# Kernel tuning notes

Hardware: AMD Instinct MI355X
Metric: run time of the kernel (lower is better)

Reference implementation:

```python
import jax, jax.numpy as jnp
import numpy as np

DIM = 1024
CTX_DIM = 1024
HEADS = 16
DIM_HEAD = 64
INNER = HEADS * DIM_HEAD
SCALE = DIM_HEAD ** -0.5


def _layer_norm(x, g, b, eps=1e-5):
    mu = x.mean(-1, keepdims=True)
    var = ((x - mu) ** 2).mean(-1, keepdims=True)
    return (x - mu) * jax.lax.rsqrt(var + eps) * g + b


def setup_inputs() -> dict:
    key = jax.random.key(0)
    ks = jax.random.split(key, 10)
    b, i, j = 2, 1024, 1024
    s = lambda fan_in: 1.0 / np.sqrt(fan_in)
    return {
        "x": jax.random.normal(ks[0], (b, i, DIM), jnp.float32),
        "context": jax.random.normal(ks[1], (b, j, CTX_DIM), jnp.float32),
        "mask": jnp.ones((b, i), dtype=bool),
        "context_mask": jnp.ones((b, j), dtype=bool),
        "ln_g": jnp.ones((DIM,), jnp.float32),
        "ln_b": jnp.zeros((DIM,), jnp.float32),
        "cln_g": jnp.ones((CTX_DIM,), jnp.float32),
        "cln_b": jnp.zeros((CTX_DIM,), jnp.float32),
        "W_qk": jax.random.normal(ks[2], (DIM, INNER), jnp.float32) * s(DIM),
        "W_cqk": jax.random.normal(ks[3], (CTX_DIM, INNER), jnp.float32) * s(CTX_DIM),
        "W_v": jax.random.normal(ks[4], (DIM, INNER), jnp.float32) * s(DIM),
        "W_cv": jax.random.normal(ks[5], (CTX_DIM, INNER), jnp.float32) * s(CTX_DIM),
        "W_out": jax.random.normal(ks[6], (INNER, DIM), jnp.float32) * s(INNER),
        "b_out": jnp.zeros((DIM,), jnp.float32),
        "W_cout": jax.random.normal(ks[7], (INNER, CTX_DIM), jnp.float32) * s(INNER),
        "b_cout": jnp.zeros((CTX_DIM,), jnp.float32),
        "W_th": jax.random.normal(ks[8], (HEADS, HEADS), jnp.float32) * s(HEADS),   # talking heads [out_h, in_h]
        "W_cth": jax.random.normal(ks[9], (HEADS, HEADS), jnp.float32) * s(HEADS),
    }


def reference(x, context, mask, context_mask, ln_g, ln_b, cln_g, cln_b,
              W_qk, W_cqk, W_v, W_cv, W_out, b_out, W_cout, b_cout, W_th, W_cth):
    b, i, _ = x.shape
    j = context.shape[1]
    xn = _layer_norm(x, ln_g, ln_b)
    cn = _layer_norm(context, cln_g, cln_b)

    split = lambda t: t.reshape(t.shape[0], t.shape[1], HEADS, DIM_HEAD).transpose(0, 2, 1, 3)  # b h n d
    qk = split(xn @ W_qk)
    cqk = split(cn @ W_cqk)
    v = split(xn @ W_v)
    cv = split(cn @ W_cv)

    sim = jnp.einsum('bhid,bhjd->bhij', qk, cqk) * SCALE

    attn_mask = mask[:, None, :, None] & context_mask[:, None, None, :]  # b 1 i j
    sim = jnp.where(attn_mask, sim, -jnp.finfo(sim.dtype).max)

    attn = jax.nn.softmax(sim, axis=-1)       # rows: x attends to context
    cattn = jax.nn.softmax(sim, axis=-2)      # cols: context attends to x

    # talking heads: 1x1 conv over head dim, weight [out_h, in_h]
    attn = jnp.einsum('bhij,gh->bgij', attn, W_th)
    cattn = jnp.einsum('bhij,gh->bgij', cattn, W_cth)

    out = jnp.einsum('bhij,bhjd->bhid', attn, cv)
    cout = jnp.einsum('bhji,bhjd->bhid', cattn, v)

    merge = lambda t: t.transpose(0, 2, 1, 3).reshape(t.shape[0], t.shape[2], INNER)
    out = merge(out) @ W_out + b_out
    cout = merge(cout) @ W_cout + b_cout
    return out, cout
```

## Files before the change

kernel.cpp:

```cpp
#include <hip/hip_runtime.h>
#include <hip/hip_bf16.h>

#define BB 2
#define SEQ 1024
#define DIMD 1024
#define NH 16
#define DH 64
#define INNERD 1024
#define SCALEF 0.125f

typedef __hip_bfloat16 bf16;
typedef __attribute__((ext_vector_type(8))) short short8;
typedef __attribute__((ext_vector_type(4))) float f32x4;

__device__ __forceinline__ float b2f(bf16 x) { return __bfloat162float(x); }
__device__ __forceinline__ bf16 f2b(float x) { return __float2bfloat16(x); }
__device__ __forceinline__ float s2f(unsigned short s) {
    return __uint_as_float(((unsigned int)s) << 16);
}
__device__ __forceinline__ unsigned short f2bs(float v) {
    bf16 t = __float2bfloat16(v);
    return *(unsigned short*)&t;
}

__device__ __forceinline__ void stf(float* p, size_t i, float v) { p[i] = v; }
__device__ __forceinline__ void stf(bf16* p, size_t i, float v) { p[i] = f2b(v); }

__device__ __forceinline__ void async16(const short* g, short* l) {
    __builtin_amdgcn_global_load_lds(
        (const __attribute__((address_space(1))) unsigned int*)(g),
        (__attribute__((address_space(3))) unsigned int*)(l), 16, 0, 0);
}

__global__ __launch_bounds__(256) void ln2_kernel(const float* __restrict__ x0,
                                                  const float* __restrict__ g0,
                                                  const float* __restrict__ b0,
                                                  bf16* __restrict__ o0,
                                                  const float* __restrict__ x1,
                                                  const float* __restrict__ g1,
                                                  const float* __restrict__ b1,
                                                  bf16* __restrict__ o1) {
    int rowg = blockIdx.x;
    int sel = rowg >= BB * SEQ;
    int row = sel ? rowg - BB * SEQ : rowg;
    const float* xr = (sel ? x1 : x0) + (size_t)row * DIMD;
    const float* g = sel ? g1 : g0;
    const float* b = sel ? b1 : b0;
    bf16* orow = (sel ? o1 : o0) + (size_t)row * DIMD;
    int tid = threadIdx.x;
    float v[4];
    float s = 0.f, s2 = 0.f;
#pragma unroll
    for (int k = 0; k < 4; ++k) {
        v[k] = xr[tid + k * 256];
        s += v[k];
        s2 += v[k] * v[k];
    }
    __shared__ float sh1[256], sh2[256];
    sh1[tid] = s; sh2[tid] = s2;
    __syncthreads();
    for (int off = 128; off > 0; off >>= 1) {
        if (tid < off) { sh1[tid] += sh1[tid + off]; sh2[tid] += sh2[tid + off]; }
        __syncthreads();
    }
    float mu = sh1[0] * (1.f / DIMD);
    float var = sh2[0] * (1.f / DIMD) - mu * mu;
    float rstd = rsqrtf(var + 1e-5f);
#pragma unroll
    for (int k = 0; k < 4; ++k) {
        int c = tid + k * 256;
        orow[c] = f2b((v[k] - mu) * rstd * g[c] + b[c]);
    }
}

__global__ __launch_bounds__(256) void transpose_w6(
    const float* __restrict__ s0, const float* __restrict__ s1,
    const float* __restrict__ s2, const float* __restrict__ s3,
    const float* __restrict__ s4, const float* __restrict__ s5,
    bf16* __restrict__ d0, bf16* __restrict__ d1, bf16* __restrict__ d2,
    bf16* __restrict__ d3, bf16* __restrict__ d4, bf16* __restrict__ d5) {
    int z = blockIdx.z;
    const float* W = z == 0 ? s0 : z == 1 ? s1 : z == 2 ? s2 : z == 3 ? s3
                     : z == 4 ? s4 : s5;
    bf16* Wt = z == 0 ? d0 : z == 1 ? d1 : z == 2 ? d2 : z == 3 ? d3
               : z == 4 ? d4 : d5;
    __shared__ float T[32][33];
    int n0 = blockIdx.x * 32, k0 = blockIdx.y * 32;
    int tx = threadIdx.x & 31, ty = threadIdx.x >> 5;
#pragma unroll
    for (int s = 0; s < 4; ++s)
        T[ty + s * 8][tx] = W[(size_t)(k0 + ty + s * 8) * 1024 + n0 + tx];
    __syncthreads();
#pragma unroll
    for (int s = 0; s < 4; ++s)
        Wt[(size_t)(n0 + ty + s * 8) * 1024 + k0 + tx] = f2b(T[tx][ty + s * 8]);
}

__global__ __launch_bounds__(256) void transpose_v2(const bf16* __restrict__ sA,
                                                    bf16* __restrict__ dA,
                                                    const bf16* __restrict__ sB,
                                                    bf16* __restrict__ dB) {
    __shared__ short T[32][34];
    int z = blockIdx.z;
    int sel = z >> 5, bh = z & 31;
    int b = bh >> 4, h = bh & 15;
    const bf16* src = sel ? sB : sA;
    bf16* dst = sel ? dB : dA;
    int n0 = blockIdx.x * 32, d0 = blockIdx.y * 32;
    int tx = threadIdx.x & 31, ty = threadIdx.x >> 5;
    const short* s = (const short*)(src + (size_t)b * SEQ * INNERD + h * DH);
    short* d = (short*)(dst + (size_t)bh * DH * SEQ);
#pragma unroll
    for (int k = 0; k < 4; ++k)
        T[ty + k * 8][tx] = s[(size_t)(n0 + ty + k * 8) * INNERD + d0 + tx];
    __syncthreads();
#pragma unroll
    for (int k = 0; k < 4; ++k)
        d[(size_t)(d0 + ty + k * 8) * SEQ + n0 + tx] = T[tx][ty + k * 8];
}

template <typename TC, bool HASBIAS, int BM, int BN, int MT, int NT, int ZS>
__global__ __launch_bounds__(256) void mfma_gemm(
    const bf16* __restrict__ A, long sA1, long sA2, int lda,
    const bf16* __restrict__ Bt, long sB1, long sB2, int ldb,
    TC* __restrict__ C, long sC1, long sC2, int ldc,
    const float* __restrict__ bias0, const float* __restrict__ bias1,
    float alpha, int K) {
    constexpr int WX = BN / (NT * 16);
    static_assert((4 / WX) * MT * 16 == BM, "BM/waves mismatch");
    static_assert(BM % 64 == 0 && BN % 64 == 0, "chunk uniformity");
    int z = blockIdx.z;
    int zb = z / ZS, zh = z % ZS;
    const short* Ag = (const short*)(A + zb * sA1 + zh * sA2);
    const short* Bg = (const short*)(Bt + zb * sB1 + zh * sB2);
    TC* Cp = C + zb * sC1 + zh * sC2;
    const float* bias = (zh == 0) ? bias0 : bias1;

    const int m0 = blockIdx.y * BM;
    const int n0 = blockIdx.x * BN;
    int tid = threadIdx.x;
    int wave = tid >> 6, lane = tid & 63;
    int wm = (wave / WX) * (MT * 16), wn = (wave % WX) * (NT * 16);
    int lrow = lane & 15, lquad = lane >> 4;

    __shared__ short S[(BM + BN) * 32];

    f32x4 acc[MT][NT] = {};

    for (int k0 = 0; k0 < K; k0 += 32) {
        constexpr int CH = (BM + BN) / 64;
#pragma unroll
        for (int ch = 0; ch < CH; ++ch) {
            int e = ch * 256 + tid;
            int r = e >> 2, c = (e & 3) * 8;
            const short* g = (r < BM)
                                 ? Ag + (size_t)(m0 + r) * lda + k0 + c
                                 : Bg + (size_t)(n0 + r - BM) * ldb + k0 + c;
            async16(g, S + (size_t)e * 8);
        }
        __syncthreads();
        short8 af[MT], bfv[NT];
#pragma unroll
        for (int mt = 0; mt < MT; ++mt)
            af[mt] = *(const short8*)(S + (wm + mt * 16 + lrow) * 32 + lquad * 8);
#pragma unroll
        for (int nt = 0; nt < NT; ++nt)
            bfv[nt] = *(const short8*)(S + (BM + wn + nt * 16 + lrow) * 32 + lquad * 8);
#pragma unroll
        for (int mt = 0; mt < MT; ++mt)
#pragma unroll
            for (int nt = 0; nt < NT; ++nt)
                acc[mt][nt] = __builtin_amdgcn_mfma_f32_16x16x32_bf16(
                    af[mt], bfv[nt], acc[mt][nt], 0, 0, 0);
        __syncthreads();
    }
#pragma unroll
    for (int mt = 0; mt < MT; ++mt) {
#pragma unroll
        for (int nt = 0; nt < NT; ++nt) {
            int col = n0 + wn + nt * 16 + lrow;
#pragma unroll
            for (int r = 0; r < 4; ++r) {
                int row = m0 + wm + mt * 16 + lquad * 4 + r;
                float v = acc[mt][nt][r] * alpha;
                if (HASBIAS) v += bias[col];
                stf(Cp, (size_t)row * ldc + col, v);
            }
        }
    }
}

__global__ __launch_bounds__(256) void qkt_stats_kernel(
    const bf16* __restrict__ qk, const bf16* __restrict__ cqk,
    bf16* __restrict__ sim16, float* __restrict__ rowPart,
    float* __restrict__ colPart, long sQ, long sS, long sP) {
    int z = blockIdx.z;
    int b = z >> 4, h = z & 15;
    const short* Ag = (const short*)(qk + b * sQ + h * DH);
    const short* Bg = (const short*)(cqk + b * sQ + h * DH);
    bf16* Cp = sim16 + b * sS + (size_t)h * SEQ * SEQ;
    rowPart += b * sP;
    colPart += b * sP;

    const int m0 = blockIdx.y * 128;
    const int n0 = blockIdx.x * 128;
    int tid = threadIdx.x;
    int wave = tid >> 6, lane = tid & 63;
    int wy = wave >> 1, wx = wave & 1;
    int wm = wy * 64, wn = wx * 64;
    int lrow = lane & 15, lquad = lane >> 4;

    __shared__ short S[256 * 32];
    __shared__ float rowLDS[128][2];
    __shared__ float colLDS[128][2];

    f32x4 acc[4][4] = {};

    for (int k0 = 0; k0 < DH; k0 += 32) {
#pragma unroll
        for (int ch = 0; ch < 4; ++ch) {
            int e = ch * 256 + tid;
            int r = e >> 2, c = (e & 3) * 8;
            const short* g = (r < 128)
                                 ? Ag + (size_t)(m0 + r) * INNERD + k0 + c
                                 : Bg + (size_t)(n0 + r - 128) * INNERD + k0 + c;
            async16(g, S + (size_t)e * 8);
        }
        __syncthreads();
        short8 af[4], bfv[4];
#pragma unroll
        for (int mt = 0; mt < 4; ++mt)
            af[mt] = *(const short8*)(S + (wm + mt * 16 + lrow) * 32 + lquad * 8);
#pragma unroll
        for (int nt = 0; nt < 4; ++nt)
            bfv[nt] = *(const short8*)(S + (128 + wn + nt * 16 + lrow) * 32 + lquad * 8);
#pragma unroll
        for (int mt = 0; mt < 4; ++mt)
#pragma unroll
            for (int nt = 0; nt < 4; ++nt)
                acc[mt][nt] = __builtin_amdgcn_mfma_f32_16x16x32_bf16(
                    af[mt], bfv[nt], acc[mt][nt], 0, 0, 0);
        __syncthreads();
    }
    float rband[16];
    float cacc[4] = {};
#pragma unroll
    for (int k = 0; k < 16; ++k) rband[k] = 0.f;
#pragma unroll
    for (int mt = 0; mt < 4; ++mt) {
#pragma unroll
        for (int nt = 0; nt < 4; ++nt) {
            int col = n0 + wn + nt * 16 + lrow;
#pragma unroll
            for (int r = 0; r < 4; ++r) {
                int row = m0 + wm + mt * 16 + lquad * 4 + r;
                unsigned short us = f2bs(acc[mt][nt][r] * SCALEF);
                *((unsigned short*)Cp + (size_t)row * SEQ + col) = us;
                float e = __expf(s2f(us));
                rband[mt * 4 + r] += e;
                cacc[nt] += e;
            }
        }
    }
#pragma unroll
    for (int m = 1; m < 16; m <<= 1)
#pragma unroll
        for (int k = 0; k < 16; ++k) rband[k] += __shfl_xor(rband[k], m, 64);
    if (lrow == 0) {
#pragma unroll
        for (int mt = 0; mt < 4; ++mt)
#pragma unroll
            for (int r = 0; r < 4; ++r)
                rowLDS[wm + mt * 16 + lquad * 4 + r][wx] = rband[mt * 4 + r];
    }
#pragma unroll
    for (int m = 16; m < 64; m <<= 1)
#pragma unroll
        for (int nt = 0; nt < 4; ++nt) cacc[nt] += __shfl_xor(cacc[nt], m, 64);
    if (lquad == 0) {
#pragma unroll
        for (int nt = 0; nt < 4; ++nt)
            colLDS[wn + nt * 16 + lrow][wy] = cacc[nt];
    }
    __syncthreads();
    if (tid < 128)
        rowPart[((size_t)h * 8 + blockIdx.x) * SEQ + m0 + tid] =
            rowLDS[tid][0] + rowLDS[tid][1];
    else
        colPart[((size_t)h * 8 + blockIdx.y) * SEQ + n0 + tid - 128] =
            colLDS[tid - 128][0] + colLDS[tid - 128][1];
}

__global__ __launch_bounds__(256) void finish_inv2_kernel(const float* __restrict__ partA,
                                                          float* __restrict__ invA,
                                                          const float* __restrict__ partB,
                                                          float* __restrict__ invB) {
    int idx = blockIdx.x * 256 + threadIdx.x;
    int h = idx >> 10, t = idx & 1023;
    float sA = 0.f, sB = 0.f;
#pragma unroll
    for (int p = 0; p < 8; ++p) {
        sA += partA[((size_t)h * 8 + p) * SEQ + t];
        sB += partB[((size_t)h * 8 + p) * SEQ + t];
    }
    invA[idx] = 1.f / sA;
    invB[idx] = 1.f / sB;
}

__global__ __launch_bounds__(256) void mix_kernel(bf16* simattn,
                                                  bf16* __restrict__ catT,
                                                  const float* __restrict__ rli,
                                                  const float* __restrict__ cli,
                                                  const float* __restrict__ Wth,
                                                  const float* __restrict__ Wcth) {
    int d = blockIdx.y * gridDim.x + blockIdx.x;
    int grp = d >> 4, s = d & 15;
    int pairIdx = grp * 8 + (s & 7);
    int half = s >> 3;
    int j0 = (2 * (pairIdx & 31) + half) * 16;
    int i0 = (pairIdx >> 5) * 16;
    int tid = threadIdx.x;
    int jl = tid & 15, il = tid >> 4;
    int i = i0 + il, j = j0 + jl;
    float sa[16] = {}, sc[16] = {};
#pragma unroll
    for (int h = 0; h < 16; ++h) {
        float s2 = b2f(simattn[((size_t)h * SEQ + i) * SEQ + j]);
        float e = __expf(s2);
        float p = e * rli[h * SEQ + i];
        float q = e * cli[h * SEQ + j];
#pragma unroll
        for (int g = 0; g < 16; ++g) {
            sa[g] += p * Wth[g * 16 + h];
            sc[g] += q * Wcth[g * 16 + h];
        }
    }
#pragma unroll
    for (int g = 0; g < 16; ++g)
        simattn[((size_t)g * SEQ + i) * SEQ + j] = f2b(sa[g]);
    __shared__ float T[16][16][17];
#pragma unroll
    for (int g = 0; g < 16; ++g) T[g][il][jl] = sc[g];
    __syncthreads();
#pragma unroll
    for (int g = 0; g < 16; ++g)
        catT[((size_t)g * SEQ + j0 + il) * SEQ + i0 + jl] = f2b(T[g][jl][il]);
}

extern "C" void kernel_launch(void* const* d_in, const int* in_sizes, int n_in,
                              void* d_out, int out_size, void* d_ws, size_t ws_size,
                              hipStream_t stream) {
    const float* x = (const float*)d_in[0];
    const float* ctx = (const float*)d_in[1];
    const float* ln_g = (const float*)d_in[4];
    const float* ln_b = (const float*)d_in[5];
    const float* cln_g = (const float*)d_in[6];
    const float* cln_b = (const float*)d_in[7];
    const float* W_qk = (const float*)d_in[8];
    const float* W_cqk = (const float*)d_in[9];
    const float* W_v = (const float*)d_in[10];
    const float* W_cv = (const float*)d_in[11];
    const float* W_out = (const float*)d_in[12];
    const float* b_out = (const float*)d_in[13];
    const float* W_cout = (const float*)d_in[14];
    const float* b_cout = (const float*)d_in[15];
    const float* W_th = (const float*)d_in[16];
    const float* W_cth = (const float*)d_in[17];
    float* out = (float*)d_out;

    char* ws = (char*)d_ws;
    size_t off = 0;
    auto alloc = [&](size_t bytes) {
        void* p = ws + off;
        off += (bytes + 255) & ~(size_t)255;
        return p;
    };
    const size_t NTOK = (size_t)BB * SEQ * DIMD;
    const size_t WSZ = (size_t)DIMD * INNERD;
    const size_t U = (size_t)NH * SEQ * SEQ;
    const long HB = (long)NH * DH * SEQ;

    bf16* xn = (bf16*)alloc(NTOK * 2);
    bf16* cn = (bf16*)alloc(NTOK * 2);
    bf16* qk = (bf16*)alloc(NTOK * 2);
    bf16* vv = (bf16*)alloc(NTOK * 2);
    bf16* cqk = (bf16*)alloc(NTOK * 2);
    bf16* cv = (bf16*)alloc(NTOK * 2);
    bf16* wqk_t = (bf16*)alloc(WSZ * 2);
    bf16* wv_t = (bf16*)alloc(WSZ * 2);
    bf16* wcqk_t = (bf16*)alloc(WSZ * 2);
    bf16* wcv_t = (bf16*)alloc(WSZ * 2);
    bf16* wout_t = (bf16*)alloc(WSZ * 2);
    bf16* wcout_t = (bf16*)alloc(WSZ * 2);
    bf16* cvT = (bf16*)alloc(NTOK * 2);
    bf16* vT = (bf16*)alloc(NTOK * 2);
    bf16* outm = xn;

    const size_t partB = (size_t)NH * 8 * SEQ * 4;
    const size_t invB = (size_t)NH * SEQ * 4;
    const size_t bigNeed = 4 * U * 2 + 2 * (2 * partB) + 2 * (2 * invB);
    bool big = (ws_size > off) && (ws_size - off >= bigNeed);

    transpose_w6<<<dim3(32, 32, 6), 256, 0, stream>>>(
        W_qk, W_v, W_cqk, W_cv, W_out, W_cout,
        wqk_t, wv_t, wcqk_t, wcv_t, wout_t, wcout_t);
    ln2_kernel<<<2 * BB * SEQ, 256, 0, stream>>>(x, ln_g, ln_b, xn,
                                                 ctx, cln_g, cln_b, cn);
    mfma_gemm<bf16, false, 128, 64, 2, 4, 2><<<dim3(16, 16, 4), 256, 0, stream>>>(
        xn, (long)NTOK, 0, DIMD,
        wqk_t, (long)(2 * WSZ), (long)WSZ, DIMD,
        qk, (long)(2 * NTOK), (long)NTOK, INNERD,
        nullptr, nullptr, 1.0f, DIMD);
    transpose_v2<<<dim3(32, 2, 64), 256, 0, stream>>>(vv, vT, cv, cvT);

    if (big) {
        bf16* sim0 = (bf16*)alloc(U * 2);
        bf16* sim1 = (bf16*)alloc(U * 2);
        bf16* cb0 = (bf16*)alloc(U * 2);
        bf16* cb1 = (bf16*)alloc(U * 2);
        float* rowPart = (float*)alloc(2 * partB);
        float* colPart = (float*)alloc(2 * partB);
        float* rowInv = (float*)alloc(2 * invB);
        float* colInv = (float*)alloc(2 * invB);

        qkt_stats_kernel<<<dim3(8, 8, 32), 256, 0, stream>>>(
            qk, cqk, sim0, rowPart, colPart,
            (long)SEQ * INNERD, (long)U, (long)NH * 8 * SEQ);
        finish_inv2_kernel<<<2 * NH * SEQ / 256, 256, 0, stream>>>(rowPart, rowInv,
                                                                   colPart, colInv);
        mix_kernel<<<dim3(SEQ / 16, SEQ / 16), 256, 0, stream>>>(
            sim0, cb0, rowInv, colInv, W_th, W_cth);
        mix_kernel<<<dim3(SEQ / 16, SEQ / 16), 256, 0, stream>>>(
            sim1, cb1, rowInv + NH * SEQ, colInv + NH * SEQ, W_th, W_cth);
        mfma_gemm<bf16, false, 64, 64, 1, 4, 16><<<dim3(1, 16, 4 * NH), 256, 0, stream>>>(
            sim0, (long)U, (long)SEQ * SEQ, SEQ,
            cvT, HB, (long)DH * SEQ, SEQ,
            outm, (long)SEQ * INNERD, (long)DH, INNERD,
            nullptr, nullptr, 1.0f, SEQ);
    } else {
        bf16* simA = (bf16*)alloc(U * 2);
        bf16* cbuf = (bf16*)alloc(U * 2);
        float* rowPart = (float*)alloc(partB);
        float* colPart = (float*)alloc(partB);
        float* rowInv = (float*)alloc(invB);
        float* colInv = (float*)alloc(invB);
        for (int b = 0; b < BB; ++b) {
            qkt_stats_kernel<<<dim3(8, 8, 16), 256, 0, stream>>>(
                qk + (size_t)b * SEQ * INNERD, cqk + (size_t)b * SEQ * INNERD,
                simA, rowPart, colPart, 0, 0, 0);
            finish_inv2_kernel<<<NH * SEQ / 256, 256, 0, stream>>>(rowPart, rowInv,
                                                                   colPart, colInv);
            mix_kernel<<<dim3(SEQ / 16, SEQ / 16), 256, 0, stream>>>(
                simA, cbuf, rowInv, colInv, W_th, W_cth);
            mfma_gemm<bf16, false, 64, 64, 1, 4, 16><<<dim3(1, 16, 2 * NH), 256, 0,
                                                       stream>>>(
                simA, (long)U, (long)SEQ * SEQ, SEQ,
                cvT + (size_t)b * HB, (long)NTOK, (long)DH * SEQ, SEQ,
                outm + (size_t)b * SEQ * INNERD, (long)NTOK, (long)DH, INNERD,
                nullptr, nullptr, 1.0f, SEQ);
        }
    }

    mfma_gemm<float, true, 128, 64, 2, 4, 2><<<dim3(16, 16, 2), 256, 0, stream>>>(
        outm, 0, (long)NTOK, INNERD, wout_t, 0, (long)WSZ, INNERD,
        out, 0, (long)NTOK, DIMD, b_out, b_cout, 1.0f, INNERD);
}
```

Before: 295.9 us.

## Merge prep kernels, deepen GEMM K-step to 64, batch mix launches

```diff
diff --git a/kernel.cpp b/kernel.cpp
--- a/kernel.cpp
+++ b/kernel.cpp
@@ -32,68 +32,65 @@
         (__attribute__((address_space(3))) unsigned int*)(l), 16, 0, 0);
 }
 
-__global__ __launch_bounds__(256) void ln2_kernel(const float* __restrict__ x0,
-                                                  const float* __restrict__ g0,
-                                                  const float* __restrict__ b0,
-                                                  bf16* __restrict__ o0,
-                                                  const float* __restrict__ x1,
-                                                  const float* __restrict__ g1,
-                                                  const float* __restrict__ b1,
-                                                  bf16* __restrict__ o1) {
-    int rowg = blockIdx.x;
-    int sel = rowg >= BB * SEQ;
-    int row = sel ? rowg - BB * SEQ : rowg;
-    const float* xr = (sel ? x1 : x0) + (size_t)row * DIMD;
-    const float* g = sel ? g1 : g0;
-    const float* b = sel ? b1 : b0;
-    bf16* orow = (sel ? o1 : o0) + (size_t)row * DIMD;
-    int tid = threadIdx.x;
-    float v[4];
-    float s = 0.f, s2 = 0.f;
-#pragma unroll
-    for (int k = 0; k < 4; ++k) {
-        v[k] = xr[tid + k * 256];
-        s += v[k];
-        s2 += v[k] * v[k];
-    }
-    __shared__ float sh1[256], sh2[256];
-    sh1[tid] = s; sh2[tid] = s2;
-    __syncthreads();
-    for (int off = 128; off > 0; off >>= 1) {
-        if (tid < off) { sh1[tid] += sh1[tid + off]; sh2[tid] += sh2[tid + off]; }
-        __syncthreads();
-    }
-    float mu = sh1[0] * (1.f / DIMD);
-    float var = sh2[0] * (1.f / DIMD) - mu * mu;
-    float rstd = rsqrtf(var + 1e-5f);
-#pragma unroll
-    for (int k = 0; k < 4; ++k) {
-        int c = tid + k * 256;
-        orow[c] = f2b((v[k] - mu) * rstd * g[c] + b[c]);
-    }
-}
-
-__global__ __launch_bounds__(256) void transpose_w6(
+__global__ __launch_bounds__(256) void prep_kernel(
     const float* __restrict__ s0, const float* __restrict__ s1,
     const float* __restrict__ s2, const float* __restrict__ s3,
     const float* __restrict__ s4, const float* __restrict__ s5,
     bf16* __restrict__ d0, bf16* __restrict__ d1, bf16* __restrict__ d2,
-    bf16* __restrict__ d3, bf16* __restrict__ d4, bf16* __restrict__ d5) {
+    bf16* __restrict__ d3, bf16* __restrict__ d4, bf16* __restrict__ d5,
+    const float* __restrict__ x0, const float* __restrict__ g0,
+    const float* __restrict__ b0, bf16* __restrict__ o0,
+    const float* __restrict__ x1, const float* __restrict__ g1,
+    const float* __restrict__ b1, bf16* __restrict__ o1) {
     int z = blockIdx.z;
-    const float* W = z == 0 ? s0 : z == 1 ? s1 : z == 2 ? s2 : z == 3 ? s3
-                     : z == 4 ? s4 : s5;
-    bf16* Wt = z == 0 ? d0 : z == 1 ? d1 : z == 2 ? d2 : z == 3 ? d3
-               : z == 4 ? d4 : d5;
-    __shared__ float T[32][33];
-    int n0 = blockIdx.x * 32, k0 = blockIdx.y * 32;
-    int tx = threadIdx.x & 31, ty = threadIdx.x >> 5;
-#pragma unroll
-    for (int s = 0; s < 4; ++s)
-        T[ty + s * 8][tx] = W[(size_t)(k0 + ty + s * 8) * 1024 + n0 + tx];
-    __syncthreads();
-#pragma unroll
-    for (int s = 0; s < 4; ++s)
-        Wt[(size_t)(n0 + ty + s * 8) * 1024 + k0 + tx] = f2b(T[tx][ty + s * 8]);
+    int tid = threadIdx.x;
+    if (z < 6) {
+        const float* W = z == 0 ? s0 : z == 1 ? s1 : z == 2 ? s2 : z == 3 ? s3
+                         : z == 4 ? s4 : s5;
+        bf16* Wt = z == 0 ? d0 : z == 1 ? d1 : z == 2 ? d2 : z == 3 ? d3
+                   : z == 4 ? d4 : d5;
+        __shared__ float T[32][33];
+        int n0 = blockIdx.x * 32, k0 = blockIdx.y * 32;
+        int tx = tid & 31, ty = tid >> 5;
+#pragma unroll
+        for (int s = 0; s < 4; ++s)
+            T[ty + s * 8][tx] = W[(size_t)(k0 + ty + s * 8) * 1024 + n0 + tx];
+        __syncthreads();
+#pragma unroll
+        for (int s = 0; s < 4; ++s)
+            Wt[(size_t)(n0 + ty + s * 8) * 1024 + k0 + tx] = f2b(T[tx][ty + s * 8]);
+    } else {
+        int rowg = (z - 6) * 1024 + blockIdx.y * 32 + blockIdx.x;
+        int sel = rowg >= BB * SEQ;
+        int row = sel ? rowg - BB * SEQ : rowg;
+        const float* xr = (sel ? x1 : x0) + (size_t)row * DIMD;
+        const float* g = sel ? g1 : g0;
+        const float* b = sel ? b1 : b0;
+        bf16* orow = (sel ? o1 : o0) + (size_t)row * DIMD;
+        float v[4];
+        float s = 0.f, s2 = 0.f;
+#pragma unroll
+        for (int k = 0; k < 4; ++k) {
+            v[k] = xr[tid + k * 256];
+            s += v[k];
+            s2 += v[k] * v[k];
+        }
+        __shared__ float sh1[256], sh2[256];
+        sh1[tid] = s; sh2[tid] = s2;
+        __syncthreads();
+        for (int off = 128; off > 0; off >>= 1) {
+            if (tid < off) { sh1[tid] += sh1[tid + off]; sh2[tid] += sh2[tid + off]; }
+            __syncthreads();
+        }
+        float mu = sh1[0] * (1.f / DIMD);
+        float var = sh2[0] * (1.f / DIMD) - mu * mu;
+        float rstd = rsqrtf(var + 1e-5f);
+#pragma unroll
+        for (int k = 0; k < 4; ++k) {
+            int c = tid + k * 256;
+            orow[c] = f2b((v[k] - mu) * rstd * g[c] + b[c]);
+        }
+    }
 }
 
 __global__ __launch_bounds__(256) void transpose_v2(const bf16* __restrict__ sA,
@@ -143,35 +140,44 @@
     int wm = (wave / WX) * (MT * 16), wn = (wave % WX) * (NT * 16);
     int lrow = lane & 15, lquad = lane >> 4;
 
-    __shared__ short S[(BM + BN) * 32];
+    __shared__ short S[2][(BM + BN) * 32];
 
     f32x4 acc[MT][NT] = {};
 
-    for (int k0 = 0; k0 < K; k0 += 32) {
+    for (int k0 = 0; k0 < K; k0 += 64) {
         constexpr int CH = (BM + BN) / 64;
 #pragma unroll
-        for (int ch = 0; ch < CH; ++ch) {
-            int e = ch * 256 + tid;
-            int r = e >> 2, c = (e & 3) * 8;
-            const short* g = (r < BM)
-                                 ? Ag + (size_t)(m0 + r) * lda + k0 + c
-                                 : Bg + (size_t)(n0 + r - BM) * ldb + k0 + c;
-            async16(g, S + (size_t)e * 8);
+        for (int half = 0; half < 2; ++half) {
+            int kh = k0 + half * 32;
+#pragma unroll
+            for (int ch = 0; ch < CH; ++ch) {
+                int e = ch * 256 + tid;
+                int r = e >> 2, c = (e & 3) * 8;
+                const short* g = (r < BM)
+                                     ? Ag + (size_t)(m0 + r) * lda + kh + c
+                                     : Bg + (size_t)(n0 + r - BM) * ldb + kh + c;
+                async16(g, S[half] + (size_t)e * 8);
+            }
         }
         __syncthreads();
-        short8 af[MT], bfv[NT];
-#pragma unroll
-        for (int mt = 0; mt < MT; ++mt)
-            af[mt] = *(const short8*)(S + (wm + mt * 16 + lrow) * 32 + lquad * 8);
-#pragma unroll
-        for (int nt = 0; nt < NT; ++nt)
-            bfv[nt] = *(const short8*)(S + (BM + wn + nt * 16 + lrow) * 32 + lquad * 8);
-#pragma unroll
-        for (int mt = 0; mt < MT; ++mt)
+#pragma unroll
+        for (int half = 0; half < 2; ++half) {
+            short8 af[MT], bfv[NT];
+#pragma unroll
+            for (int mt = 0; mt < MT; ++mt)
+                af[mt] = *(const short8*)(S[half] + (wm + mt * 16 + lrow) * 32 +
+                                          lquad * 8);
 #pragma unroll
             for (int nt = 0; nt < NT; ++nt)
-                acc[mt][nt] = __builtin_amdgcn_mfma_f32_16x16x32_bf16(
-                    af[mt], bfv[nt], acc[mt][nt], 0, 0, 0);
+                bfv[nt] = *(const short8*)(S[half] + (BM + wn + nt * 16 + lrow) * 32 +
+                                           lquad * 8);
+#pragma unroll
+            for (int mt = 0; mt < MT; ++mt)
+#pragma unroll
+                for (int nt = 0; nt < NT; ++nt)
+                    acc[mt][nt] = __builtin_amdgcn_mfma_f32_16x16x32_bf16(
+                        af[mt], bfv[nt], acc[mt][nt], 0, 0, 0);
+        }
         __syncthreads();
     }
 #pragma unroll
@@ -210,37 +216,42 @@
     int wm = wy * 64, wn = wx * 64;
     int lrow = lane & 15, lquad = lane >> 4;
 
-    __shared__ short S[256 * 32];
+    __shared__ short S[2][256 * 32];
     __shared__ float rowLDS[128][2];
     __shared__ float colLDS[128][2];
 
     f32x4 acc[4][4] = {};
 
-    for (int k0 = 0; k0 < DH; k0 += 32) {
+#pragma unroll
+    for (int half = 0; half < 2; ++half) {
+        int kh = half * 32;
 #pragma unroll
         for (int ch = 0; ch < 4; ++ch) {
             int e = ch * 256 + tid;
             int r = e >> 2, c = (e & 3) * 8;
             const short* g = (r < 128)
-                                 ? Ag + (size_t)(m0 + r) * INNERD + k0 + c
-                                 : Bg + (size_t)(n0 + r - 128) * INNERD + k0 + c;
-            async16(g, S + (size_t)e * 8);
-        }
-        __syncthreads();
+                                 ? Ag + (size_t)(m0 + r) * INNERD + kh + c
+                                 : Bg + (size_t)(n0 + r - 128) * INNERD + kh + c;
+            async16(g, S[half] + (size_t)e * 8);
+        }
+    }
+    __syncthreads();
+#pragma unroll
+    for (int half = 0; half < 2; ++half) {
         short8 af[4], bfv[4];
 #pragma unroll
         for (int mt = 0; mt < 4; ++mt)
-            af[mt] = *(const short8*)(S + (wm + mt * 16 + lrow) * 32 + lquad * 8);
+            af[mt] = *(const short8*)(S[half] + (wm + mt * 16 + lrow) * 32 + lquad * 8);
 #pragma unroll
         for (int nt = 0; nt < 4; ++nt)
-            bfv[nt] = *(const short8*)(S + (128 + wn + nt * 16 + lrow) * 32 + lquad * 8);
+            bfv[nt] = *(const short8*)(S[half] + (128 + wn + nt * 16 + lrow) * 32 +
+                                       lquad * 8);
 #pragma unroll
         for (int mt = 0; mt < 4; ++mt)
 #pragma unroll
             for (int nt = 0; nt < 4; ++nt)
                 acc[mt][nt] = __builtin_amdgcn_mfma_f32_16x16x32_bf16(
                     af[mt], bfv[nt], acc[mt][nt], 0, 0, 0);
-        __syncthreads();
     }
     float rband[16];
     float cacc[4] = {};
@@ -312,7 +323,13 @@
                                                   const float* __restrict__ rli,
                                                   const float* __restrict__ cli,
                                                   const float* __restrict__ Wth,
-                                                  const float* __restrict__ Wcth) {
+                                                  const float* __restrict__ Wcth,
+                                                  long sS, long sI) {
+    int zb = blockIdx.z;
+    simattn += zb * sS;
+    catT += zb * sS;
+    rli += zb * sI;
+    cli += zb * sI;
     int d = blockIdx.y * gridDim.x + blockIdx.x;
     int grp = d >> 4, s = d & 15;
     int pairIdx = grp * 8 + (s & 7);
@@ -401,11 +418,10 @@
     const size_t bigNeed = 4 * U * 2 + 2 * (2 * partB) + 2 * (2 * invB);
     bool big = (ws_size > off) && (ws_size - off >= bigNeed);
 
-    transpose_w6<<<dim3(32, 32, 6), 256, 0, stream>>>(
+    prep_kernel<<<dim3(32, 32, 10), 256, 0, stream>>>(
         W_qk, W_v, W_cqk, W_cv, W_out, W_cout,
-        wqk_t, wv_t, wcqk_t, wcv_t, wout_t, wcout_t);
-    ln2_kernel<<<2 * BB * SEQ, 256, 0, stream>>>(x, ln_g, ln_b, xn,
-                                                 ctx, cln_g, cln_b, cn);
+        wqk_t, wv_t, wcqk_t, wcv_t, wout_t, wcout_t,
+        x, ln_g, ln_b, xn, ctx, cln_g, cln_b, cn);
     mfma_gemm<bf16, false, 128, 64, 2, 4, 2><<<dim3(16, 16, 4), 256, 0, stream>>>(
         xn, (long)NTOK, 0, DIMD,
         wqk_t, (long)(2 * WSZ), (long)WSZ, DIMD,
@@ -422,16 +438,15 @@
         float* colPart = (float*)alloc(2 * partB);
         float* rowInv = (float*)alloc(2 * invB);
         float* colInv = (float*)alloc(2 * invB);
+        (void)sim1; (void)cb1;
 
         qkt_stats_kernel<<<dim3(8, 8, 32), 256, 0, stream>>>(
             qk, cqk, sim0, rowPart, colPart,
             (long)SEQ * INNERD, (long)U, (long)NH * 8 * SEQ);
         finish_inv2_kernel<<<2 * NH * SEQ / 256, 256, 0, stream>>>(rowPart, rowInv,
                                                                    colPart, colInv);
-        mix_kernel<<<dim3(SEQ / 16, SEQ / 16), 256, 0, stream>>>(
-            sim0, cb0, rowInv, colInv, W_th, W_cth);
-        mix_kernel<<<dim3(SEQ / 16, SEQ / 16), 256, 0, stream>>>(
-            sim1, cb1, rowInv + NH * SEQ, colInv + NH * SEQ, W_th, W_cth);
+        mix_kernel<<<dim3(SEQ / 16, SEQ / 16, 2), 256, 0, stream>>>(
+            sim0, cb0, rowInv, colInv, W_th, W_cth, (long)U, (long)NH * SEQ);
         mfma_gemm<bf16, false, 64, 64, 1, 4, 16><<<dim3(1, 16, 4 * NH), 256, 0, stream>>>(
             sim0, (long)U, (long)SEQ * SEQ, SEQ,
             cvT, HB, (long)DH * SEQ, SEQ,
@@ -450,8 +465,8 @@
                 simA, rowPart, colPart, 0, 0, 0);
             finish_inv2_kernel<<<NH * SEQ / 256, 256, 0, stream>>>(rowPart, rowInv,
                                                                    colPart, colInv);
-            mix_kernel<<<dim3(SEQ / 16, SEQ / 16), 256, 0, stream>>>(
-                simA, cbuf, rowInv, colInv, W_th, W_cth);
+            mix_kernel<<<dim3(SEQ / 16, SEQ / 16, 1), 256, 0, stream>>>(
+                simA, cbuf, rowInv, colInv, W_th, W_cth, 0, 0);
             mfma_gemm<bf16, false, 64, 64, 1, 4, 16><<<dim3(1, 16, 2 * NH), 256, 0,
                                                        stream>>>(
                 simA, (long)U, (long)SEQ * SEQ, SEQ,
```

Result: faster. 287.6 us (-2.8%).
